# Optimization experiments

Hardware: AMD Instinct MI355X
Metric: run time of the kernel (lower is better)

Reference implementation:

```python
import jax, jax.numpy as jnp
import numpy as np

N_NODES = 100000
N_EDGES = 1200000
D_FEAT = 64
THETA = (1.0, -0.8, 0.4, -0.1)  # polynomial coefficients, k = len(THETA)


def setup_inputs() -> dict:
    key = jax.random.key(0)
    k1, k2, k3 = jax.random.split(key, 3)
    feat = jax.random.normal(k1, (N_NODES, D_FEAT), dtype=jnp.float32)
    src = jax.random.randint(k2, (N_EDGES,), 0, N_NODES, dtype=jnp.int32)
    dst = jax.random.randint(k3, (N_EDGES,), 0, N_NODES, dtype=jnp.int32)
    return {"feat": feat, "src": src, "dst": dst}


def reference(feat, src, dst):
    # in-degrees: number of incoming edges per node (clamped to >= 1)
    deg = jax.ops.segment_sum(jnp.ones((N_EDGES,), feat.dtype), dst, num_segments=N_NODES)
    d_invsqrt = jnp.clip(deg, 1.0, None) ** -0.5  # [N]
    d = d_invsqrt[:, None]  # [N, 1]

    h = THETA[0] * feat
    for k in range(1, len(THETA)):
        # unnLaplacian: feat - D^{-1/2} A^T (D^{-1/2} feat)  (copy_u / sum over edges)
        msg = (feat * d)[src]                                   # [E, F] gather
        agg = jax.ops.segment_sum(msg, dst, num_segments=N_NODES)  # [N, F] scatter-add
        feat = feat - agg * d
        h = h + THETA[k] * feat
    return h
```

## Files before the change

### kernel.cpp

```cpp
#include <hip/hip_runtime.h>

#define D_FEAT 64
#define BSHIFT 8
#define MAXB 512
#define CHUNK 8192

__device__ inline unsigned short f2bf(float f) {
    unsigned u = __float_as_uint(f);
    unsigned r = u + 0x7fffu + ((u >> 16) & 1u);
    return (unsigned short)(r >> 16);
}
__device__ inline float bflo(unsigned w) { return __uint_as_float(w << 16); }
__device__ inline float bfhi(unsigned w) { return __uint_as_float(w & 0xffff0000u); }

__device__ inline void unpack8(uint4 u, float* v) {
    v[0] = bflo(u.x); v[1] = bfhi(u.x);
    v[2] = bflo(u.y); v[3] = bfhi(u.y);
    v[4] = bflo(u.z); v[5] = bfhi(u.z);
    v[6] = bflo(u.w); v[7] = bfhi(u.w);
}
__device__ inline uint4 pack8(const float* v) {
    uint4 u;
    u.x = (unsigned)f2bf(v[0]) | ((unsigned)f2bf(v[1]) << 16);
    u.y = (unsigned)f2bf(v[2]) | ((unsigned)f2bf(v[3]) << 16);
    u.z = (unsigned)f2bf(v[4]) | ((unsigned)f2bf(v[5]) << 16);
    u.w = (unsigned)f2bf(v[6]) | ((unsigned)f2bf(v[7]) << 16);
    return u;
}

__global__ void tobf16_kernel(const float4* __restrict__ f, uint4* __restrict__ fb, int n8) {
    int i = blockIdx.x * blockDim.x + threadIdx.x;
    if (i >= n8) return;
    float4 a = f[(size_t)i * 2];
    float4 b = f[(size_t)i * 2 + 1];
    float v[8] = {a.x, a.y, a.z, a.w, b.x, b.y, b.z, b.w};
    fb[i] = pack8(v);
}

__global__ void bhist_kernel(const int* __restrict__ dst, int* __restrict__ mat,
                             int nE, int P, int nblk) {
    __shared__ int lh[MAXB];
    for (int i = threadIdx.x; i < P; i += blockDim.x) lh[i] = 0;
    __syncthreads();
    int s = blockIdx.x * CHUNK;
    int e1 = s + CHUNK; if (e1 > nE) e1 = nE;
    for (int e = s + threadIdx.x; e < e1; e += blockDim.x)
        atomicAdd(&lh[dst[e] >> BSHIFT], 1);
    __syncthreads();
    for (int i = threadIdx.x; i < P; i += blockDim.x)
        mat[i * nblk + blockIdx.x] = lh[i];
}

__global__ void scan1_kernel(const int* __restrict__ in, int* __restrict__ out,
                             int* __restrict__ bsums, int n) {
    __shared__ int tmp[256];
    int tid = threadIdx.x;
    int i = blockIdx.x * 256 + tid;
    int v = (i < n) ? in[i] : 0;
    tmp[tid] = v;
    __syncthreads();
    for (int off = 1; off < 256; off <<= 1) {
        int t2 = 0;
        if (tid >= off) t2 = tmp[tid - off];
        __syncthreads();
        tmp[tid] += t2;
        __syncthreads();
    }
    if (i < n) out[i] = tmp[tid] - v;
    if (tid == 255) bsums[blockIdx.x] = tmp[255];
}

__global__ void scan2_kernel(int* __restrict__ bsums, int nb) {
    __shared__ int tmp[512];
    int tid = threadIdx.x;
    int v = (tid < nb) ? bsums[tid] : 0;
    tmp[tid] = v;
    __syncthreads();
    for (int off = 1; off < 512; off <<= 1) {
        int t2 = 0;
        if (tid >= off) t2 = tmp[tid - off];
        __syncthreads();
        tmp[tid] += t2;
        __syncthreads();
    }
    if (tid < nb) bsums[tid] = tmp[tid] - v;
}

__global__ void scan3add_kernel(int* __restrict__ matS, const int* __restrict__ bsums,
                                int* __restrict__ bucket_ptr, int n, int nblk,
                                int P, int nE) {
    int i = blockIdx.x * 256 + threadIdx.x;
    if (i < n) {
        int v = matS[i] + bsums[blockIdx.x];
        matS[i] = v;
        if (i % nblk == 0) bucket_ptr[i / nblk] = v;
    }
    if (i == 0) bucket_ptr[P] = nE;
}

__global__ void scatter_part_kernel(const int* __restrict__ src, const int* __restrict__ dst,
                                    const int* __restrict__ matS, int2* __restrict__ part,
                                    int nE, int P, int nblk) {
    __shared__ int cur[MAXB];
    for (int i = threadIdx.x; i < P; i += blockDim.x)
        cur[i] = matS[i * nblk + blockIdx.x];
    __syncthreads();
    int s = blockIdx.x * CHUNK;
    int e1 = s + CHUNK; if (e1 > nE) e1 = nE;
    for (int e = s + threadIdx.x; e < e1; e += blockDim.x) {
        int t = dst[e];
        int pos = atomicAdd(&cur[t >> BSHIFT], 1);
        part[pos] = make_int2(src[e], t);
    }
}

__global__ void bucket_csr_kernel(const int2* __restrict__ part,
                                  const int* __restrict__ bucket_ptr,
                                  int* __restrict__ row_ptr, int* __restrict__ row_end,
                                  float* __restrict__ dv, int* __restrict__ esrc, int nN) {
    __shared__ int hist[256];
    __shared__ int cur[256];
    __shared__ int scanT[256];
    int b = blockIdx.x;
    int tid = threadIdx.x;
    int bp0 = bucket_ptr[b], bp1 = bucket_ptr[b + 1];
    hist[tid] = 0;
    __syncthreads();
    for (int e = bp0 + tid; e < bp1; e += 256)
        atomicAdd(&hist[part[e].y & 255], 1);
    __syncthreads();
    int v = hist[tid];
    scanT[tid] = v;
    __syncthreads();
    for (int off = 1; off < 256; off <<= 1) {
        int t2 = 0;
        if (tid >= off) t2 = scanT[tid - off];
        __syncthreads();
        scanT[tid] += t2;
        __syncthreads();
    }
    int startv = scanT[tid] - v;
    cur[tid] = startv;
    int node = (b << BSHIFT) + tid;
    if (node < nN) {
        float fc = (float)(v < 1 ? 1 : v);
        dv[node] = rsqrtf(fc);
        row_ptr[node] = bp0 + startv;
        row_end[node] = bp0 + startv + v;
    }
    __syncthreads();
    for (int e = bp0 + tid; e < bp1; e += 256) {
        int2 p = part[e];
        int rank = atomicAdd(&cur[p.y & 255], 1);
        esrc[bp0 + rank] = p.x;
    }
}

__global__ void poly_kernel(const uint4* __restrict__ fb_in, uint4* __restrict__ fb_out,
                            const int* __restrict__ row_ptr, const int* __restrict__ row_end,
                            const int* __restrict__ esrc, const float* __restrict__ d,
                            const uint4* __restrict__ fb0, const uint4* __restrict__ fb1,
                            const float4* __restrict__ f0f, float4* __restrict__ h,
                            int final_step, int nN) {
    int wave = (blockIdx.x * blockDim.x + threadIdx.x) >> 6;
    int lane = threadIdx.x & 63;
    int sub  = lane >> 3;
    int q    = lane & 7;
    int t    = wave * 8 + sub;
    bool valid = (t < nN);
    if (!valid) t = nN - 1;

    int r0 = row_ptr[t], r1 = row_end[t];
    if (!valid) r1 = r0;

    float acc[8];
#pragma unroll
    for (int c = 0; c < 8; ++c) acc[c] = 0.0f;

    for (int j0 = r0; j0 < r1; j0 += 8) {
        int jj = j0 + q;
        int jc = jj < r1 ? jj : (r1 - 1);
        int   sq = esrc[jc];
        float dq = d[sq];
        int m = r1 - j0; if (m > 8) m = 8;
        for (int i = 0; i < 8; i += 4) {
            if (i >= m) break;
#pragma unroll
            for (int u = 0; u < 4; ++u) {
                int bl = (sub << 3) + i + u;
                int   sb = __shfl(sq, bl, 64);
                float ds = __shfl(dq, bl, 64);
                ds = (i + u < m) ? ds : 0.0f;
                uint4 fv = fb_in[(size_t)sb * 8 + q];
                float v[8];
                unpack8(fv, v);
#pragma unroll
                for (int c = 0; c < 8; ++c) acc[c] = fmaf(v[c], ds, acc[c]);
            }
        }
    }

    if (!valid) return;
    size_t idx = (size_t)t * 8 + q;
    float dt = d[t];
    float fo[8];
    unpack8(fb_in[idx], fo);
    float fn[8];
#pragma unroll
    for (int c = 0; c < 8; ++c) fn[c] = fo[c] - acc[c] * dt;

    if (!final_step) {
        fb_out[idx] = pack8(fn);
    } else {
        float f1v[8];
        unpack8(fb1[idx], f1v);
        float f0v[8];
        if (f0f) {
            float4 a = f0f[(size_t)t * 16 + q * 2];
            float4 b = f0f[(size_t)t * 16 + q * 2 + 1];
            f0v[0] = a.x; f0v[1] = a.y; f0v[2] = a.z; f0v[3] = a.w;
            f0v[4] = b.x; f0v[5] = b.y; f0v[6] = b.z; f0v[7] = b.w;
        } else {
            unpack8(fb0[idx], f0v);
        }
        float hv[8];
#pragma unroll
        for (int c = 0; c < 8; ++c)
            hv[c] = f0v[c] - 0.8f * f1v[c] + 0.4f * fo[c] - 0.1f * fn[c];
        h[(size_t)t * 16 + q * 2]     = make_float4(hv[0], hv[1], hv[2], hv[3]);
        h[(size_t)t * 16 + q * 2 + 1] = make_float4(hv[4], hv[5], hv[6], hv[7]);
    }
}

extern "C" void kernel_launch(void* const* d_in, const int* in_sizes, int n_in,
                              void* d_out, int out_size, void* d_ws, size_t ws_size,
                              hipStream_t stream) {
    const float* feat = (const float*)d_in[0];
    const int*   src  = (const int*)d_in[1];
    const int*   dst  = (const int*)d_in[2];
    float*       h    = (float*)d_out;

    const int nN = in_sizes[0] / D_FEAT;
    const int nE = in_sizes[1];

    const int P    = (nN + 255) >> 8;
    const int nblk = (nE + CHUNK - 1) / CHUNK;
    const int n    = P * nblk;
    const int nb   = (n + 255) / 256;

    auto align = [](size_t x) { return (x + 255) & ~(size_t)255; };
    char* ws = (char*)d_ws;
    size_t off = 0;
    int*   mat        = (int*)(ws + off);   off += align((size_t)n * 4);
    int*   matS       = (int*)(ws + off);   off += align((size_t)n * 4);
    int*   bsums      = (int*)(ws + off);   off += align(512 * 4);
    int*   bucket_ptr = (int*)(ws + off);   off += align((size_t)(P + 1) * 4);
    int*   row_ptr    = (int*)(ws + off);   off += align((size_t)nN * 4);
    int*   row_end    = (int*)(ws + off);   off += align((size_t)nN * 4);
    float* dv         = (float*)(ws + off); off += align((size_t)nN * 4);
    int2*  part       = (int2*)(ws + off);  off += align((size_t)nE * 8);
    int*   esrc       = (int*)(ws + off);   off += align((size_t)nE * 4);
    size_t fbBytes = (size_t)nN * D_FEAT * 2;
    uint4* fb0        = (uint4*)(ws + off); off += align(fbBytes);
    uint4* fb1        = (uint4*)(ws + off); off += align(fbBytes);
    uint4* fb2;
    const float4* f0f;
    if (ws_size >= off + fbBytes) {
        fb2 = (uint4*)(ws + off);
        f0f = (const float4*)feat;
    } else {
        fb2 = (uint4*)d_in[0];
        f0f = nullptr;
    }

    const int n8 = nN * 8;
    tobf16_kernel      <<<(n8 + 255) / 256, 256, 0, stream>>>((const float4*)feat, fb0, n8);
    bhist_kernel       <<<nblk, 256, 0, stream>>>(dst, mat, nE, P, nblk);
    scan1_kernel       <<<nb, 256, 0, stream>>>(mat, matS, bsums, n);
    scan2_kernel       <<<1, 512, 0, stream>>>(bsums, nb);
    scan3add_kernel    <<<nb, 256, 0, stream>>>(matS, bsums, bucket_ptr, n, nblk, P, nE);
    scatter_part_kernel<<<nblk, 256, 0, stream>>>(src, dst, matS, part, nE, P, nblk);
    bucket_csr_kernel  <<<P, 256, 0, stream>>>(part, bucket_ptr, row_ptr, row_end,
                                               dv, esrc, nN);

    long long waves = ((long long)nN + 7) / 8;
    int polyBlocks = (int)((waves * 64 + 255) / 256);
    poly_kernel<<<polyBlocks, 256, 0, stream>>>(fb0, fb1, row_ptr, row_end, esrc, dv,
                                                nullptr, nullptr, nullptr, nullptr, 0, nN);
    poly_kernel<<<polyBlocks, 256, 0, stream>>>(fb1, fb2, row_ptr, row_end, esrc, dv,
                                                nullptr, nullptr, nullptr, nullptr, 0, nN);
    poly_kernel<<<polyBlocks, 256, 0, stream>>>(fb2, nullptr, row_ptr, row_end, esrc, dv,
                                                fb0, fb1, f0f, (float4*)h, 1, nN);
}
```

Baseline: 216.8 us.

## Fuse preprocessing kernels, pack edge pairs to 32-bit, prefetch neighbor indices

Merges the bf16 conversion and bucket histogram into one launch and halves CHUNK. Packs each partitioned edge into a single 32-bit word (src<<8 | low dst bits) instead of an int2, halving partition traffic. In the aggregation loop it software-prefetches the next group's source indices and degrees, and in the final step it stores h non-temporally. The final step now reads the first term from bf16 rather than fp32, which lowers precision of the theta0 term. The packing assumes src fits in 24 bits.

```diff
diff --git a/kernel.cpp b/kernel.cpp
--- a/kernel.cpp
+++ b/kernel.cpp
@@ -3,7 +3,9 @@
 #define D_FEAT 64
 #define BSHIFT 8
 #define MAXB 512
-#define CHUNK 8192
+#define CHUNK 4096
+
+typedef float nfloat4 __attribute__((ext_vector_type(4)));
 
 __device__ inline unsigned short f2bf(float f) {
     unsigned u = __float_as_uint(f);
@@ -28,27 +30,30 @@
     return u;
 }
 
-__global__ void tobf16_kernel(const float4* __restrict__ f, uint4* __restrict__ fb, int n8) {
-    int i = blockIdx.x * blockDim.x + threadIdx.x;
-    if (i >= n8) return;
-    float4 a = f[(size_t)i * 2];
-    float4 b = f[(size_t)i * 2 + 1];
-    float v[8] = {a.x, a.y, a.z, a.w, b.x, b.y, b.z, b.w};
-    fb[i] = pack8(v);
-}
-
-__global__ void bhist_kernel(const int* __restrict__ dst, int* __restrict__ mat,
-                             int nE, int P, int nblk) {
+__global__ void pre_kernel(const int* __restrict__ dst, int* __restrict__ mat,
+                           const float4* __restrict__ f, uint4* __restrict__ fb,
+                           int nE, int P, int nblk, int n8) {
     __shared__ int lh[MAXB];
-    for (int i = threadIdx.x; i < P; i += blockDim.x) lh[i] = 0;
-    __syncthreads();
-    int s = blockIdx.x * CHUNK;
-    int e1 = s + CHUNK; if (e1 > nE) e1 = nE;
-    for (int e = s + threadIdx.x; e < e1; e += blockDim.x)
-        atomicAdd(&lh[dst[e] >> BSHIFT], 1);
-    __syncthreads();
-    for (int i = threadIdx.x; i < P; i += blockDim.x)
-        mat[i * nblk + blockIdx.x] = lh[i];
+    int b = blockIdx.x;
+    if (b < nblk) {
+        for (int i = threadIdx.x; i < P; i += blockDim.x) lh[i] = 0;
+        __syncthreads();
+        int s = b * CHUNK;
+        int e1 = s + CHUNK; if (e1 > nE) e1 = nE;
+        for (int e = s + threadIdx.x; e < e1; e += blockDim.x)
+            atomicAdd(&lh[dst[e] >> BSHIFT], 1);
+        __syncthreads();
+        for (int i = threadIdx.x; i < P; i += blockDim.x)
+            mat[i * nblk + b] = lh[i];
+    } else {
+        int i = (b - nblk) * 256 + threadIdx.x;
+        if (i < n8) {
+            float4 a = f[(size_t)i * 2];
+            float4 c = f[(size_t)i * 2 + 1];
+            float v[8] = {a.x, a.y, a.z, a.w, c.x, c.y, c.z, c.w};
+            fb[i] = pack8(v);
+        }
+    }
 }
 
 __global__ void scan1_kernel(const int* __restrict__ in, int* __restrict__ out,
@@ -99,7 +104,7 @@
 }
 
 __global__ void scatter_part_kernel(const int* __restrict__ src, const int* __restrict__ dst,
-                                    const int* __restrict__ matS, int2* __restrict__ part,
+                                    const int* __restrict__ matS, unsigned* __restrict__ part,
                                     int nE, int P, int nblk) {
     __shared__ int cur[MAXB];
     for (int i = threadIdx.x; i < P; i += blockDim.x)
@@ -110,11 +115,11 @@
     for (int e = s + threadIdx.x; e < e1; e += blockDim.x) {
         int t = dst[e];
         int pos = atomicAdd(&cur[t >> BSHIFT], 1);
-        part[pos] = make_int2(src[e], t);
-    }
-}
-
-__global__ void bucket_csr_kernel(const int2* __restrict__ part,
+        part[pos] = ((unsigned)src[e] << 8) | (unsigned)(t & 255);
+    }
+}
+
+__global__ void bucket_csr_kernel(const unsigned* __restrict__ part,
                                   const int* __restrict__ bucket_ptr,
                                   int* __restrict__ row_ptr, int* __restrict__ row_end,
                                   float* __restrict__ dv, int* __restrict__ esrc, int nN) {
@@ -127,7 +132,7 @@
     hist[tid] = 0;
     __syncthreads();
     for (int e = bp0 + tid; e < bp1; e += 256)
-        atomicAdd(&hist[part[e].y & 255], 1);
+        atomicAdd(&hist[part[e] & 255u], 1);
     __syncthreads();
     int v = hist[tid];
     scanT[tid] = v;
@@ -150,9 +155,9 @@
     }
     __syncthreads();
     for (int e = bp0 + tid; e < bp1; e += 256) {
-        int2 p = part[e];
-        int rank = atomicAdd(&cur[p.y & 255], 1);
-        esrc[bp0 + rank] = p.x;
+        unsigned p = part[e];
+        int rank = atomicAdd(&cur[p & 255u], 1);
+        esrc[bp0 + rank] = (int)(p >> 8);
     }
 }
 
@@ -160,8 +165,7 @@
                             const int* __restrict__ row_ptr, const int* __restrict__ row_end,
                             const int* __restrict__ esrc, const float* __restrict__ d,
                             const uint4* __restrict__ fb0, const uint4* __restrict__ fb1,
-                            const float4* __restrict__ f0f, float4* __restrict__ h,
-                            int final_step, int nN) {
+                            float* __restrict__ h, int final_step, int nN) {
     int wave = (blockIdx.x * blockDim.x + threadIdx.x) >> 6;
     int lane = threadIdx.x & 63;
     int sub  = lane >> 3;
@@ -177,20 +181,43 @@
 #pragma unroll
     for (int c = 0; c < 8; ++c) acc[c] = 0.0f;
 
-    for (int j0 = r0; j0 < r1; j0 += 8) {
-        int jj = j0 + q;
-        int jc = jj < r1 ? jj : (r1 - 1);
-        int   sq = esrc[jc];
-        float dq = d[sq];
+    int   sq = 0;
+    float dq = 0.0f;
+    if (r0 < r1) {
+        int jc = r0 + q; if (jc > r1 - 1) jc = r1 - 1;
+        sq = esrc[jc];
+        dq = d[sq];
+    }
+    int j0 = r0;
+    while (j0 < r1) {
+        int jn = j0 + 8;
+        int   sq_n = 0;
+        float dq_n = 0.0f;
+        if (jn < r1) {
+            int jc = jn + q; if (jc > r1 - 1) jc = r1 - 1;
+            sq_n = esrc[jc];
+            dq_n = d[sq_n];
+        }
         int m = r1 - j0; if (m > 8) m = 8;
-        for (int i = 0; i < 8; i += 4) {
-            if (i >= m) break;
-#pragma unroll
-            for (int u = 0; u < 4; ++u) {
-                int bl = (sub << 3) + i + u;
+#pragma unroll
+        for (int u = 0; u < 4; ++u) {
+            int bl = (sub << 3) + u;
+            int   sb = __shfl(sq, bl, 64);
+            float ds = __shfl(dq, bl, 64);
+            ds = (u < m) ? ds : 0.0f;
+            uint4 fv = fb_in[(size_t)sb * 8 + q];
+            float v[8];
+            unpack8(fv, v);
+#pragma unroll
+            for (int c = 0; c < 8; ++c) acc[c] = fmaf(v[c], ds, acc[c]);
+        }
+        if (m > 4) {
+#pragma unroll
+            for (int u = 4; u < 8; ++u) {
+                int bl = (sub << 3) + u;
                 int   sb = __shfl(sq, bl, 64);
                 float ds = __shfl(dq, bl, 64);
-                ds = (i + u < m) ? ds : 0.0f;
+                ds = (u < m) ? ds : 0.0f;
                 uint4 fv = fb_in[(size_t)sb * 8 + q];
                 float v[8];
                 unpack8(fv, v);
@@ -198,6 +225,7 @@
                 for (int c = 0; c < 8; ++c) acc[c] = fmaf(v[c], ds, acc[c]);
             }
         }
+        sq = sq_n; dq = dq_n; j0 = jn;
     }
 
     if (!valid) return;
@@ -215,20 +243,16 @@
         float f1v[8];
         unpack8(fb1[idx], f1v);
         float f0v[8];
-        if (f0f) {
-            float4 a = f0f[(size_t)t * 16 + q * 2];
-            float4 b = f0f[(size_t)t * 16 + q * 2 + 1];
-            f0v[0] = a.x; f0v[1] = a.y; f0v[2] = a.z; f0v[3] = a.w;
-            f0v[4] = b.x; f0v[5] = b.y; f0v[6] = b.z; f0v[7] = b.w;
-        } else {
-            unpack8(fb0[idx], f0v);
-        }
+        unpack8(fb0[idx], f0v);
         float hv[8];
 #pragma unroll
         for (int c = 0; c < 8; ++c)
             hv[c] = f0v[c] - 0.8f * f1v[c] + 0.4f * fo[c] - 0.1f * fn[c];
-        h[(size_t)t * 16 + q * 2]     = make_float4(hv[0], hv[1], hv[2], hv[3]);
-        h[(size_t)t * 16 + q * 2 + 1] = make_float4(hv[4], hv[5], hv[6], hv[7]);
+        nfloat4 h0 = {hv[0], hv[1], hv[2], hv[3]};
+        nfloat4 h1 = {hv[4], hv[5], hv[6], hv[7]};
+        nfloat4* hp = (nfloat4*)(h + (size_t)t * 64 + q * 8);
+        __builtin_nontemporal_store(h0, hp);
+        __builtin_nontemporal_store(h1, hp + 1);
     }
 }
 
@@ -251,31 +275,29 @@
     auto align = [](size_t x) { return (x + 255) & ~(size_t)255; };
     char* ws = (char*)d_ws;
     size_t off = 0;
-    int*   mat        = (int*)(ws + off);   off += align((size_t)n * 4);
-    int*   matS       = (int*)(ws + off);   off += align((size_t)n * 4);
-    int*   bsums      = (int*)(ws + off);   off += align(512 * 4);
-    int*   bucket_ptr = (int*)(ws + off);   off += align((size_t)(P + 1) * 4);
-    int*   row_ptr    = (int*)(ws + off);   off += align((size_t)nN * 4);
-    int*   row_end    = (int*)(ws + off);   off += align((size_t)nN * 4);
-    float* dv         = (float*)(ws + off); off += align((size_t)nN * 4);
-    int2*  part       = (int2*)(ws + off);  off += align((size_t)nE * 8);
-    int*   esrc       = (int*)(ws + off);   off += align((size_t)nE * 4);
+    int*      mat        = (int*)(ws + off);      off += align((size_t)n * 4);
+    int*      matS       = (int*)(ws + off);      off += align((size_t)n * 4);
+    int*      bsums      = (int*)(ws + off);      off += align(512 * 4);
+    int*      bucket_ptr = (int*)(ws + off);      off += align((size_t)(P + 1) * 4);
+    int*      row_ptr    = (int*)(ws + off);      off += align((size_t)nN * 4);
+    int*      row_end    = (int*)(ws + off);      off += align((size_t)nN * 4);
+    float*    dv         = (float*)(ws + off);    off += align((size_t)nN * 4);
+    unsigned* part       = (unsigned*)(ws + off); off += align((size_t)nE * 4);
+    int*      esrc       = (int*)(ws + off);      off += align((size_t)nE * 4);
     size_t fbBytes = (size_t)nN * D_FEAT * 2;
-    uint4* fb0        = (uint4*)(ws + off); off += align(fbBytes);
-    uint4* fb1        = (uint4*)(ws + off); off += align(fbBytes);
-    uint4* fb2;
-    const float4* f0f;
+    uint4*    fb0        = (uint4*)(ws + off);    off += align(fbBytes);
+    uint4*    fb1        = (uint4*)(ws + off);    off += align(fbBytes);
+    uint4*    fb2;
     if (ws_size >= off + fbBytes) {
         fb2 = (uint4*)(ws + off);
-        f0f = (const float4*)feat;
     } else {
         fb2 = (uint4*)d_in[0];
-        f0f = nullptr;
     }
 
     const int n8 = nN * 8;
-    tobf16_kernel      <<<(n8 + 255) / 256, 256, 0, stream>>>((const float4*)feat, fb0, n8);
-    bhist_kernel       <<<nblk, 256, 0, stream>>>(dst, mat, nE, P, nblk);
+    const int tb = (n8 + 255) / 256;
+    pre_kernel         <<<nblk + tb, 256, 0, stream>>>(dst, mat, (const float4*)feat,
+                                                       fb0, nE, P, nblk, n8);
     scan1_kernel       <<<nb, 256, 0, stream>>>(mat, matS, bsums, n);
     scan2_kernel       <<<1, 512, 0, stream>>>(bsums, nb);
     scan3add_kernel    <<<nb, 256, 0, stream>>>(matS, bsums, bucket_ptr, n, nblk, P, nE);
@@ -286,9 +308,9 @@
     long long waves = ((long long)nN + 7) / 8;
     int polyBlocks = (int)((waves * 64 + 255) / 256);
     poly_kernel<<<polyBlocks, 256, 0, stream>>>(fb0, fb1, row_ptr, row_end, esrc, dv,
-                                                nullptr, nullptr, nullptr, nullptr, 0, nN);
+                                                nullptr, nullptr, nullptr, 0, nN);
     poly_kernel<<<polyBlocks, 256, 0, stream>>>(fb1, fb2, row_ptr, row_end, esrc, dv,
-                                                nullptr, nullptr, nullptr, nullptr, 0, nN);
+                                                nullptr, nullptr, nullptr, 0, nN);
     poly_kernel<<<polyBlocks, 256, 0, stream>>>(fb2, nullptr, row_ptr, row_end, esrc, dv,
-                                                fb0, fb1, f0f, (float4*)h, 1, nN);
-}
+                                                fb0, fb1, h, 1, nN);
+}
```

Measured after the change: 204.8 us. 5.5% less time.
